# Kernel tuning notes

Hardware: AMD Instinct MI355X
Metric: run time of the kernel (lower is better)

## Reference

```python
import jax, jax.numpy as jnp
import numpy as np

B, S, E = 4, 2048, 512
H, D = 8, 64  # n_head, attn_dim


def setup_inputs() -> dict:
    key = jax.random.key(0)
    ks = jax.random.split(key, 12)
    scale = 0.02
    return {
        "input_q": jax.random.normal(ks[0], (B, S, E), dtype=jnp.float32),
        "input_k": jax.random.normal(ks[1], (B, S, E), dtype=jnp.float32),
        "input_v": jax.random.normal(ks[2], (B, S, E), dtype=jnp.float32),
        "mask": jax.random.randint(ks[3], (B, S, S), 0, 2, dtype=jnp.int32),
        "wq": jax.random.normal(ks[4], (E, H * D), dtype=jnp.float32) * scale,
        "bq": jnp.zeros((H * D,), dtype=jnp.float32),
        "wk": jax.random.normal(ks[5], (E, H * D), dtype=jnp.float32) * scale,
        "bk": jnp.zeros((H * D,), dtype=jnp.float32),
        "wv": jax.random.normal(ks[6], (E, H * D), dtype=jnp.float32) * scale,
        "bv": jnp.zeros((H * D,), dtype=jnp.float32),
        "wo": jax.random.normal(ks[7], (H * D, E), dtype=jnp.float32) * scale,
        "bo": jnp.zeros((E,), dtype=jnp.float32),
    }


def reference(input_q, input_k, input_v, mask, wq, bq, wk, bk, wv, bv, wo, bo):
    b, lq, _ = input_q.shape
    lk = input_k.shape[1]
    # projections -> [b, len, H, D] -> [b, H, len, D]
    q = (input_q @ wq + bq).reshape(b, lq, H, D).transpose(0, 2, 1, 3)
    k = (input_k @ wk + bk).reshape(b, lk, H, D).transpose(0, 2, 1, 3)
    v = (input_v @ wv + bv).reshape(b, lk, H, D).transpose(0, 2, 1, 3)
    # raw scores [b, H, lq, lk]
    score = jnp.einsum("bhqd,bhkd->bhqk", q, k)
    # NOTE: original masks with -1e9 BEFORE dividing by sqrt(attn_dim)
    score = jnp.where(mask[:, None, :, :] == 0, jnp.float32(-1e9), score)
    attn = jax.nn.softmax(score / jnp.sqrt(jnp.float32(D)), axis=-1)
    out = jnp.einsum("bhqk,bhkd->bqhd", attn, v).reshape(b, lq, H * D)
    return out @ wo + bo
```

## Files before the change

kernel.cpp:

```cpp
#include <hip/hip_runtime.h>
#include <hip/hip_bf16.h>
#include <hip/hip_fp16.h>
#include <stdint.h>

#define Bc 4
#define Sc 2048
#define Ec 512
#define Hc 8
#define Dc 64
#define HDc 512

typedef __attribute__((ext_vector_type(8))) short bf16x8;
typedef __attribute__((ext_vector_type(2))) _Float16 f16x2;
typedef __attribute__((ext_vector_type(4))) _Float16 f16x4;
typedef __attribute__((ext_vector_type(8))) _Float16 f16x8;
typedef __attribute__((ext_vector_type(4))) float f32x4;
typedef __attribute__((ext_vector_type(16))) float f32x16;
typedef unsigned int u32;

__device__ __forceinline__ unsigned short f2bf(float x) {
    union { float f; unsigned u; } v; v.f = x;
    unsigned r = v.u + 0x7FFFu + ((v.u >> 16) & 1u);
    return (unsigned short)(r >> 16);
}

__device__ __forceinline__ unsigned pkbf2(float a, float b) {
    float2 f; f.x = a; f.y = b;
    __hip_bfloat162 h = __float22bfloat162_rn(f);
    union { __hip_bfloat162 h2; unsigned u; } u; u.h2 = h;
    return u.u;
}

__device__ __forceinline__ unsigned short f2h(float x) {
    return __half_as_ushort(__float2half_rn(x));
}

__device__ __forceinline__ unsigned pkh2(float a, float b) {
    union { __half2 h2; unsigned u; } u;
    u.h2 = __floats2half2_rn(a, b);
    return u.u;
}

__device__ __forceinline__ uint4 pack8(float4 a, float4 b) {
    uint4 v;
    v.x = pkbf2(a.x, a.y); v.y = pkbf2(a.z, a.w);
    v.z = pkbf2(b.x, b.y); v.w = pkbf2(b.z, b.w);
    return v;
}

__device__ __forceinline__ void gload_lds(const void* g, void* l) {
    __builtin_amdgcn_global_load_lds(
        (const __attribute__((address_space(1))) u32*)g,
        (__attribute__((address_space(3))) u32*)l,
        16, 0, 0);
}

__global__ __launch_bounds__(256) void prep(
    const int* __restrict__ mask, unsigned long long* __restrict__ bits,
    const float* __restrict__ W0, const float* __restrict__ W1,
    const float* __restrict__ W2, const float* __restrict__ W3,
    unsigned short* __restrict__ Wt,
    const float* __restrict__ Xq, const float* __restrict__ Xk,
    const float* __restrict__ Xv, unsigned short* __restrict__ Xb)
{
    const int blk = blockIdx.x;
    __shared__ float t[64][65];
    if (blk < 256) {
        const int z = blk >> 6;
        const float* W = z == 0 ? W0 : (z == 1 ? W1 : (z == 2 ? W2 : W3));
        unsigned short* O = Wt + (size_t)z * Ec * HDc;
        const int k0 = ((blk >> 3) & 7) * 64, n0 = (blk & 7) * 64;
#pragma unroll
        for (int i = 0; i < 16; i++) {
            int idx = threadIdx.x + 256 * i;
            int kr = idx >> 6, nc = idx & 63;
            t[nc][kr] = W[(size_t)(k0 + kr) * HDc + n0 + nc];
        }
        __syncthreads();
#pragma unroll
        for (int i = 0; i < 16; i++) {
            int idx = threadIdx.x + 256 * i;
            int nr = idx >> 6, kc = idx & 63;
            O[(size_t)(n0 + nr) * Ec + k0 + kc] = f2bf(t[nr][kc]);
        }
    } else if (blk < 2304) {
        const int lane = threadIdx.x & 63;
        int wave = ((blk - 256) * 256 + (int)threadIdx.x) >> 6;
        const int nwaves = (2048 * 256) >> 6;
        const int nwords = (Bc * Sc * Sc) / 64;
        for (int w = wave; w < nwords; w += nwaves) {
            int m = mask[(size_t)w * 64 + lane];
            unsigned long long b = __ballot(m != 0);
            if (lane == 0) bits[w] = b;
        }
    } else {
        const int zi = blk - 2304;
        const int z = zi >> 11, wi = zi & 2047;
        const float* X = z == 0 ? Xq : (z == 1 ? Xk : Xv);
        const size_t off = ((size_t)wi * 256 + threadIdx.x) * 8;
        const float4* p = (const float4*)(X + off);
        float4 f0 = p[0], f1 = p[1];
        *(uint4*)(Xb + (size_t)z * 4194304 + off) = pack8(f0, f1);
    }
}

__global__ __launch_bounds__(256) void proj_gemm(
    const unsigned short* __restrict__ Xb, const unsigned short* __restrict__ Wt,
    const float* __restrict__ bq, const float* __restrict__ bk, const float* __restrict__ bv,
    unsigned short* __restrict__ Oq, unsigned short* __restrict__ Ok,
    unsigned short* __restrict__ Vt)
{
    const int z = blockIdx.z;
    const unsigned short* Xz = Xb + (size_t)z * 4194304;
    const unsigned short* Bt = Wt + (size_t)z * Ec * HDc;
    const float* bias = z == 0 ? bq : (z == 1 ? bk : bv);

    const int n0 = blockIdx.x * 128;
    const int m0 = blockIdx.y * 128;
    const int tid = threadIdx.x, lane = tid & 63, w = tid >> 6;
    const int c = lane & 15, quad = lane >> 4;
    const int wm = w & 1, wn = w >> 1;

    __shared__ unsigned short As[128 * 64];
    __shared__ unsigned short Bs[128 * 64];

    f32x4 acc[4][4];
#pragma unroll
    for (int i = 0; i < 4; i++)
#pragma unroll
        for (int j = 0; j < 4; j++) acc[i][j] = (f32x4){0.f, 0.f, 0.f, 0.f};

    for (int k0 = 0; k0 < Ec; k0 += 64) {
        __syncthreads();
#pragma unroll
        for (int jj = 0; jj < 4; jj++) {
            int rb = w * 32 + jj * 8;
            int row = rb + (lane >> 3);
            int dg = (lane & 7) ^ (row & 7);
            gload_lds(Bt + (size_t)(n0 + row) * Ec + k0 + dg * 8, &Bs[rb * 64]);
            gload_lds(Xz + (size_t)(m0 + row) * Ec + k0 + dg * 8, &As[rb * 64]);
        }
        __syncthreads();
#pragma unroll
        for (int ks = 0; ks < 2; ks++) {
            int kg = ks * 4 + quad;
            bf16x8 af[4], bfr[4];
#pragma unroll
            for (int mt = 0; mt < 4; mt++) {
                int row = wm * 64 + mt * 16 + c;
                af[mt] = *(const bf16x8*)&As[row * 64 + ((kg ^ (row & 7)) * 8)];
            }
#pragma unroll
            for (int nt = 0; nt < 4; nt++) {
                int row = wn * 64 + nt * 16 + c;
                bfr[nt] = *(const bf16x8*)&Bs[row * 64 + ((kg ^ (row & 7)) * 8)];
            }
            if (z < 2) {
#pragma unroll
                for (int mt = 0; mt < 4; mt++)
#pragma unroll
                    for (int nt = 0; nt < 4; nt++)
                        acc[mt][nt] = __builtin_amdgcn_mfma_f32_16x16x32_bf16(af[mt], bfr[nt], acc[mt][nt], 0, 0, 0);
            } else {
#pragma unroll
                for (int mt = 0; mt < 4; mt++)
#pragma unroll
                    for (int nt = 0; nt < 4; nt++)
                        acc[mt][nt] = __builtin_amdgcn_mfma_f32_16x16x32_bf16(bfr[nt], af[mt], acc[mt][nt], 0, 0, 0);
            }
        }
    }

    if (z < 2) {
        unsigned short* O = z == 0 ? Oq : Ok;
        const float qs = z == 0 ? 0.125f : 1.0f;
#pragma unroll
        for (int mt = 0; mt < 4; mt++)
#pragma unroll
            for (int r = 0; r < 4; r++) {
                int gm = m0 + wm * 64 + mt * 16 + quad * 4 + r;
#pragma unroll
                for (int nt = 0; nt < 4; nt++) {
                    int gn = n0 + wn * 64 + nt * 16 + c;
                    O[(size_t)gm * HDc + gn] = f2bf((acc[mt][nt][r] + bias[gn]) * qs);
                }
            }
    } else {
#pragma unroll
        for (int mt = 0; mt < 4; mt++) {
            int gm = m0 + wm * 64 + mt * 16 + c;
            int bb = gm >> 11, sPos = gm & (Sc - 1);
#pragma unroll
            for (int nt = 0; nt < 4; nt++)
#pragma unroll
                for (int r = 0; r < 4; r++) {
                    int ng = n0 + wn * 64 + nt * 16 + quad * 4 + r;
                    int hh = ng >> 6, d = ng & 63;
                    Vt[((size_t)(bb * Hc + hh) * Dc + d) * Sc + sPos] = f2h(acc[mt][nt][r] + bias[ng]);
                }
        }
    }
}

__global__ __launch_bounds__(256, 2) void attn_kernel(
    const unsigned short* __restrict__ Qb, const unsigned short* __restrict__ Kb,
    const unsigned short* __restrict__ Vt, const unsigned long long* __restrict__ Mb,
    unsigned short* __restrict__ Ob)
{
    const int flat = blockIdx.x + 16 * blockIdx.y + 128 * blockIdx.z;
    const int hb = flat & 7;
    const int qt = (flat >> 3) & 15;
    const int b  = flat >> 7;
    const int q0 = qt * 128;
    const int tid = threadIdx.x, lane = tid & 63, w = tid >> 6;
    const int l31 = lane & 31, hf = lane >> 5;

    __shared__ unsigned short Ks[2][64 * 64];
    __shared__ unsigned short Vs[2][64 * 64];

    const int qg = q0 + w * 32 + l31;
    const size_t qoff = ((size_t)b * Sc + qg) * HDc + hb * Dc;

    bf16x8 qf[4];
#pragma unroll
    for (int s4 = 0; s4 < 4; s4++)
        qf[s4] = *(const bf16x8*)(Qb + qoff + s4 * 16 + hf * 8);

    const unsigned long long* mr = Mb + ((size_t)b * Sc + qg) * (Sc / 64);
    const size_t kbase = ((size_t)b * Sc) * HDc + hb * Dc;
    const size_t vbase = ((size_t)(b * Hc + hb)) * Dc * Sc;

    f32x16 o[2];
#pragma unroll
    for (int i = 0; i < 16; i++) { o[0][i] = 0.f; o[1][i] = 0.f; }
    float os[4] = {0.f, 0.f, 0.f, 0.f};
    const f16x2 one2 = {(_Float16)1.0f, (_Float16)1.0f};

    auto stage = [&](int kt, int buf) {
#pragma unroll
        for (int j = 0; j < 2; j++) {
            int rb = w * 16 + j * 8;
            int row = rb + (lane >> 3);
            int dg = (lane & 7) ^ (row & 7);
            gload_lds(Kb + kbase + (size_t)(kt * 64 + row) * HDc + dg * 8, &Ks[buf][rb * 64]);
            gload_lds(Vt + vbase + (size_t)row * Sc + kt * 64 + dg * 8, &Vs[buf][rb * 64]);
        }
    };

    stage(0, 0);
    for (int kt = 0; kt < Sc / 64; kt++) {
        const int cur = kt & 1;
        unsigned long long mw = mr[kt];
        __syncthreads();
        if (kt + 1 < Sc / 64) stage(kt + 1, cur ^ 1);

        u32 P16[2][8];
#pragma unroll
        for (int a = 0; a < 2; a++) {
            f32x16 s;
#pragma unroll
            for (int i = 0; i < 16; i++) s[i] = 0.f;
            const int t = a * 32 + l31;
#pragma unroll
            for (int s4 = 0; s4 < 4; s4++) {
                bf16x8 kf = *(const bf16x8*)&Ks[cur][t * 64 + (((2 * s4 + hf) ^ (t & 7)) * 8)];
                s = __builtin_amdgcn_mfma_f32_32x32x16_bf16(kf, qf[s4], s, 0, 0, 0);
            }
            u32 mwa = (a == 0) ? (u32)mw : (u32)(mw >> 32);
            int mq = (int)(mwa >> (4 * hf));
#pragma unroll
            for (int g = 0; g < 4; g++) {
                float p[4];
#pragma unroll
                for (int r = 0; r < 4; r++) {
                    const int pos = 8 * g + r;
                    int keep = __builtin_amdgcn_sbfe(mq, pos, 1);
                    float e = __expf(s[4 * g + r]);
                    p[r] = __int_as_float(__float_as_int(e) & keep);
                }
                u32 u0 = pkh2(p[0], p[1]);
                u32 u1 = pkh2(p[2], p[3]);
                P16[a][2 * g + 0] = u0;
                P16[a][2 * g + 1] = u1;
                union { u32 u; f16x2 h; } d0, d1;
                d0.u = u0; d1.u = u1;
                os[g] = __builtin_amdgcn_fdot2(d0.h, one2, os[g], false);
                os[g] = __builtin_amdgcn_fdot2(d1.h, one2, os[g], false);
            }
        }

        u32 pw[4][4];
#pragma unroll
        for (int s4 = 0; s4 < 4; s4++) {
            const int a = s4 >> 1, base = 4 * (s4 & 1);
#pragma unroll
            for (int pp = 0; pp < 2; pp++) {
                u32 A0 = P16[a][base + pp];
                u32 B1 = P16[a][base + 2 + pp];
                u32 sent = hf ? A0 : B1;
                u32 got = (u32)__shfl_xor((int)sent, 32, 64);
                pw[s4][pp]     = hf ? got : A0;
                pw[s4][2 + pp] = hf ? B1  : got;
            }
        }
#pragma unroll
        for (int s4 = 0; s4 < 4; s4++) {
            union { u32 u[4]; f16x8 v; } pf;
            pf.u[0] = pw[s4][0]; pf.u[1] = pw[s4][1];
            pf.u[2] = pw[s4][2]; pf.u[3] = pw[s4][3];
#pragma unroll
            for (int dt = 0; dt < 2; dt++) {
                const int d = dt * 32 + l31;
                f16x8 vf = *(const f16x8*)&Vs[cur][d * 64 + (((2 * s4 + hf) ^ (d & 7)) * 8)];
                o[dt] = __builtin_amdgcn_mfma_f32_32x32x16_f16(vf, pf.v, o[dt], 0, 0, 0);
            }
        }
    }

    float osum = os[0] + os[1] + os[2] + os[3];
    osum += __shfl_xor(osum, 32, 64);
    const float inv = 1.0f / osum;

#pragma unroll
    for (int dt = 0; dt < 2; dt++)
#pragma unroll
        for (int g = 0; g < 4; g++) {
            const int d = dt * 32 + 8 * g + 4 * hf;
            uint2 pk;
            pk.x = pkbf2(o[dt][4 * g + 0] * inv, o[dt][4 * g + 1] * inv);
            pk.y = pkbf2(o[dt][4 * g + 2] * inv, o[dt][4 * g + 3] * inv);
            *(uint2*)(Ob + qoff + d) = pk;
        }
}

__global__ __launch_bounds__(256) void out_gemm(
    const unsigned short* __restrict__ Ab, const unsigned short* __restrict__ Bt,
    const float* __restrict__ bias, float* __restrict__ Out)
{
    const int n0 = blockIdx.x * 128;
    const int m0 = blockIdx.y * 64;
    const int tid = threadIdx.x, lane = tid & 63, w = tid >> 6;
    const int c = lane & 15, quad = lane >> 4;
    const int wm = w & 1, wn = w >> 1;

    __shared__ unsigned short As[64 * 64];
    __shared__ unsigned short Bs[128 * 64];

    f32x4 acc[2][4];
#pragma unroll
    for (int i = 0; i < 2; i++)
#pragma unroll
        for (int j = 0; j < 4; j++) acc[i][j] = (f32x4){0.f, 0.f, 0.f, 0.f};

    for (int k0 = 0; k0 < HDc; k0 += 64) {
        __syncthreads();
#pragma unroll
        for (int jj = 0; jj < 4; jj++) {
            int rb = w * 32 + jj * 8;
            int row = rb + (lane >> 3);
            int dg = (lane & 7) ^ (row & 7);
            gload_lds(Bt + (size_t)(n0 + row) * Ec + k0 + dg * 8, &Bs[rb * 64]);
        }
#pragma unroll
        for (int jj = 0; jj < 2; jj++) {
            int rb = w * 16 + jj * 8;
            int row = rb + (lane >> 3);
            int dg = (lane & 7) ^ (row & 7);
            gload_lds(Ab + (size_t)(m0 + row) * HDc + k0 + dg * 8, &As[rb * 64]);
        }
        __syncthreads();
#pragma unroll
        for (int ks = 0; ks < 2; ks++) {
            int kg = ks * 4 + quad;
            bf16x8 af[2], bfr[4];
#pragma unroll
            for (int mt = 0; mt < 2; mt++) {
                int row = wm * 32 + mt * 16 + c;
                af[mt] = *(const bf16x8*)&As[row * 64 + ((kg ^ (row & 7)) * 8)];
            }
#pragma unroll
            for (int nt = 0; nt < 4; nt++) {
                int row = wn * 64 + nt * 16 + c;
                bfr[nt] = *(const bf16x8*)&Bs[row * 64 + ((kg ^ (row & 7)) * 8)];
            }
#pragma unroll
            for (int mt = 0; mt < 2; mt++)
#pragma unroll
                for (int nt = 0; nt < 4; nt++)
                    acc[mt][nt] = __builtin_amdgcn_mfma_f32_16x16x32_bf16(af[mt], bfr[nt], acc[mt][nt], 0, 0, 0);
        }
    }
#pragma unroll
    for (int mt = 0; mt < 2; mt++)
#pragma unroll
        for (int r = 0; r < 4; r++) {
            int gm = m0 + wm * 32 + mt * 16 + quad * 4 + r;
#pragma unroll
            for (int nt = 0; nt < 4; nt++) {
                int gn = n0 + wn * 64 + nt * 16 + c;
                Out[(size_t)gm * Ec + gn] = acc[mt][nt][r] + bias[gn];
            }
        }
}

extern "C" void kernel_launch(void* const* d_in, const int* in_sizes, int n_in,
                              void* d_out, int out_size, void* d_ws, size_t ws_size,
                              hipStream_t stream)
{
    const float* xq = (const float*)d_in[0];
    const float* xk = (const float*)d_in[1];
    const float* xv = (const float*)d_in[2];
    const int* mask = (const int*)d_in[3];
    const float* wq = (const float*)d_in[4];
    const float* bq = (const float*)d_in[5];
    const float* wk = (const float*)d_in[6];
    const float* bk = (const float*)d_in[7];
    const float* wv = (const float*)d_in[8];
    const float* bv = (const float*)d_in[9];
    const float* wo = (const float*)d_in[10];
    const float* bo = (const float*)d_in[11];
    float* out = (float*)d_out;

    char* ws = (char*)d_ws;
    const size_t MB = 1024 * 1024;
    unsigned short* qb = (unsigned short*)(ws + 0 * MB);
    unsigned short* kb = (unsigned short*)(ws + 8 * MB);
    unsigned short* vt = (unsigned short*)(ws + 16 * MB);
    unsigned short* xb = (unsigned short*)(ws + 24 * MB);
    unsigned short* ab = (unsigned short*)(ws + 24 * MB);
    unsigned long long* mb = (unsigned long long*)(ws + 48 * MB);
    unsigned short* wt = (unsigned short*)(ws + 50 * MB);

    hipLaunchKernelGGL(prep, dim3(8448), dim3(256), 0, stream,
                       mask, mb, wq, wk, wv, wo, wt, xq, xk, xv, xb);

    hipLaunchKernelGGL(proj_gemm, dim3(4, 64, 3), dim3(256), 0, stream,
                       xb, wt, bq, bk, bv, qb, kb, vt);

    hipLaunchKernelGGL(attn_kernel, dim3(16, 8, 4), dim3(256), 0, stream,
                       qb, kb, vt, mb, ab);

    hipLaunchKernelGGL(out_gemm, dim3(4, 128), dim3(256), 0, stream,
                       ab, wt + 3 * (size_t)Ec * HDc, bo, out);
}
```

Before: 273.7 us.

## Split attention key range across warp pairs and merge partial outputs via LDS

Each attention block now covers 64 queries instead of 128, and its four warps form two halves that each process half of the key sequence for the same 32-query groups. Partial outputs and row sums are reduced through shared memory at the end. The grid doubles and the launch bound moves to 4 blocks per CU, aiming at better occupancy and latency hiding. In exchange the K/V double-buffering is dropped: each tile is loaded synchronously, with two barriers per iteration. The final merge also adds LDS traffic.

Measured after the change: 269.2 us, median of 2. Within noise of the previous version (-1.6%).

```diff
diff --git a/kernel.cpp b/kernel.cpp
--- a/kernel.cpp
+++ b/kernel.cpp
@@ -202,23 +202,26 @@
     }
 }
 
-__global__ __launch_bounds__(256, 2) void attn_kernel(
+__global__ __launch_bounds__(256, 4) void attn_kernel(
     const unsigned short* __restrict__ Qb, const unsigned short* __restrict__ Kb,
     const unsigned short* __restrict__ Vt, const unsigned long long* __restrict__ Mb,
     unsigned short* __restrict__ Ob)
 {
-    const int flat = blockIdx.x + 16 * blockIdx.y + 128 * blockIdx.z;
+    const int flat = blockIdx.x + 32 * blockIdx.y + 256 * blockIdx.z;
     const int hb = flat & 7;
-    const int qt = (flat >> 3) & 15;
-    const int b  = flat >> 7;
-    const int q0 = qt * 128;
+    const int qt = (flat >> 3) & 31;
+    const int b  = flat >> 8;
+    const int q0 = qt * 64;
     const int tid = threadIdx.x, lane = tid & 63, w = tid >> 6;
     const int l31 = lane & 31, hf = lane >> 5;
-
-    __shared__ unsigned short Ks[2][64 * 64];
-    __shared__ unsigned short Vs[2][64 * 64];
-
-    const int qg = q0 + w * 32 + l31;
+    const int half = w >> 1;
+    const int qgrp = w & 1;
+
+    __shared__ unsigned short SM[16384];
+    unsigned short* KsH = SM + half * 4096;
+    unsigned short* VsH = SM + 8192 + half * 4096;
+
+    const int qg = q0 + qgrp * 32 + l31;
     const size_t qoff = ((size_t)b * Sc + qg) * HDc + hb * Dc;
 
     bf16x8 qf[4];
@@ -236,34 +239,33 @@
     float os[4] = {0.f, 0.f, 0.f, 0.f};
     const f16x2 one2 = {(_Float16)1.0f, (_Float16)1.0f};
 
-    auto stage = [&](int kt, int buf) {
-#pragma unroll
-        for (int j = 0; j < 2; j++) {
-            int rb = w * 16 + j * 8;
+    auto stage = [&](int t) {
+#pragma unroll
+        for (int jj = 0; jj < 4; jj++) {
+            int rb = qgrp * 32 + jj * 8;
             int row = rb + (lane >> 3);
             int dg = (lane & 7) ^ (row & 7);
-            gload_lds(Kb + kbase + (size_t)(kt * 64 + row) * HDc + dg * 8, &Ks[buf][rb * 64]);
-            gload_lds(Vt + vbase + (size_t)row * Sc + kt * 64 + dg * 8, &Vs[buf][rb * 64]);
+            gload_lds(Kb + kbase + (size_t)(t * 64 + row) * HDc + dg * 8, &KsH[rb * 64]);
+            gload_lds(Vt + vbase + (size_t)row * Sc + t * 64 + dg * 8, &VsH[rb * 64]);
         }
     };
 
-    stage(0, 0);
-    for (int kt = 0; kt < Sc / 64; kt++) {
-        const int cur = kt & 1;
-        unsigned long long mw = mr[kt];
-        __syncthreads();
-        if (kt + 1 < Sc / 64) stage(kt + 1, cur ^ 1);
+    for (int i = 0; i < 16; i++) {
+        const int t = half * 16 + i;
+        unsigned long long mw = mr[t];
+        stage(t);
+        __syncthreads();
 
         u32 P16[2][8];
 #pragma unroll
         for (int a = 0; a < 2; a++) {
             f32x16 s;
 #pragma unroll
-            for (int i = 0; i < 16; i++) s[i] = 0.f;
-            const int t = a * 32 + l31;
+            for (int i2 = 0; i2 < 16; i2++) s[i2] = 0.f;
+            const int tk = a * 32 + l31;
 #pragma unroll
             for (int s4 = 0; s4 < 4; s4++) {
-                bf16x8 kf = *(const bf16x8*)&Ks[cur][t * 64 + (((2 * s4 + hf) ^ (t & 7)) * 8)];
+                bf16x8 kf = *(const bf16x8*)&KsH[tk * 64 + (((2 * s4 + hf) ^ (tk & 7)) * 8)];
                 s = __builtin_amdgcn_mfma_f32_32x32x16_bf16(kf, qf[s4], s, 0, 0, 0);
             }
             u32 mwa = (a == 0) ? (u32)mw : (u32)(mw >> 32);
@@ -311,26 +313,44 @@
 #pragma unroll
             for (int dt = 0; dt < 2; dt++) {
                 const int d = dt * 32 + l31;
-                f16x8 vf = *(const f16x8*)&Vs[cur][d * 64 + (((2 * s4 + hf) ^ (d & 7)) * 8)];
+                f16x8 vf = *(const f16x8*)&VsH[d * 64 + (((2 * s4 + hf) ^ (d & 7)) * 8)];
                 o[dt] = __builtin_amdgcn_mfma_f32_32x32x16_f16(vf, pf.v, o[dt], 0, 0, 0);
             }
         }
+        __syncthreads();
     }
 
     float osum = os[0] + os[1] + os[2] + os[3];
     osum += __shfl_xor(osum, 32, 64);
-    const float inv = 1.0f / osum;
-
-#pragma unroll
-    for (int dt = 0; dt < 2; dt++)
-#pragma unroll
-        for (int g = 0; g < 4; g++) {
-            const int d = dt * 32 + 8 * g + 4 * hf;
-            uint2 pk;
-            pk.x = pkbf2(o[dt][4 * g + 0] * inv, o[dt][4 * g + 1] * inv);
-            pk.y = pkbf2(o[dt][4 * g + 2] * inv, o[dt][4 * g + 3] * inv);
-            *(uint2*)(Ob + qoff + d) = pk;
-        }
+
+    float* mbuf = (float*)SM;
+    if (half == 1) {
+        float* mp = mbuf + (qgrp * 64 + lane) * 34;
+#pragma unroll
+        for (int dt = 0; dt < 2; dt++)
+#pragma unroll
+            for (int i = 0; i < 16; i++) mp[dt * 16 + i] = o[dt][i];
+        mp[32] = osum;
+    }
+    __syncthreads();
+    if (half == 0) {
+        const float* mp = mbuf + (qgrp * 64 + lane) * 34;
+#pragma unroll
+        for (int dt = 0; dt < 2; dt++)
+#pragma unroll
+            for (int i = 0; i < 16; i++) o[dt][i] += mp[dt * 16 + i];
+        const float inv = 1.0f / (osum + mp[32]);
+#pragma unroll
+        for (int dt = 0; dt < 2; dt++)
+#pragma unroll
+            for (int g = 0; g < 4; g++) {
+                const int d = dt * 32 + 8 * g + 4 * hf;
+                uint2 pk;
+                pk.x = pkbf2(o[dt][4 * g + 0] * inv, o[dt][4 * g + 1] * inv);
+                pk.y = pkbf2(o[dt][4 * g + 2] * inv, o[dt][4 * g + 3] * inv);
+                *(uint2*)(Ob + qoff + d) = pk;
+            }
+    }
 }
 
 __global__ __launch_bounds__(256) void out_gemm(
@@ -437,7 +457,7 @@
     hipLaunchKernelGGL(proj_gemm, dim3(4, 64, 3), dim3(256), 0, stream,
                        xb, wt, bq, bk, bv, qb, kb, vt);
 
-    hipLaunchKernelGGL(attn_kernel, dim3(16, 8, 4), dim3(256), 0, stream,
+    hipLaunchKernelGGL(attn_kernel, dim3(32, 8, 4), dim3(256), 0, stream,
                        qb, kb, vt, mb, ab);
 
     hipLaunchKernelGGL(out_gemm, dim3(4, 128), dim3(256), 0, stream,
```
